# Performance work log

Measured on AMD Instinct MI355X. Metric: run time of the kernel, lower is better.

Reference implementation:

```python
import jax, jax.numpy as jnp
import numpy as np
from jax import lax

K = 3
K2 = K * K
EPS = 1e-5


def conv3x3(x, w, b=None):
    # x [B,C,H,W], w [O,C,3,3], padding=1, stride=1
    out = lax.conv_general_dilated(x, w, (1, 1), [(1, 1), (1, 1)],
                                   dimension_numbers=('NCHW', 'OIHW', 'NCHW'))
    if b is not None:
        out = out + b[None, :, None, None]
    return out


def deform_conv(x, w_off, b_off, w_mod, b_mod, w):
    # DCNv2-style deformable conv, k=3, stride=1, pad=1, dilation=1, no bias.
    B, C, H, W = x.shape
    O = w.shape[0]
    off = conv3x3(x, w_off, b_off).reshape(B, K2, 2, H, W)   # (dy,dx) per tap
    mod = 2.0 * jax.nn.sigmoid(conv3x3(x, w_mod, b_mod))      # [B,9,H,W]
    dy, dx = off[:, :, 0], off[:, :, 1]

    ky = (jnp.arange(K) - 1).astype(x.dtype)
    base_y = jnp.repeat(ky, K)   # [9]
    base_x = jnp.tile(ky, K)     # [9]
    ii = jnp.arange(H, dtype=x.dtype)[:, None]
    jj = jnp.arange(W, dtype=x.dtype)[None, :]
    py = ii[None, None] + base_y[None, :, None, None] + dy   # [B,9,H,W]
    px = jj[None, None] + base_x[None, :, None, None] + dx

    def sample(xb, pyb, pxb):
        # xb [C,H,W]; pyb/pxb [9,H,W] -> [C,9,H,W], bilinear w/ zero pad
        y0 = jnp.floor(pyb)
        x0 = jnp.floor(pxb)
        wy = pyb - y0
        wx = pxb - x0
        flat = xb.reshape(C, -1)
        acc = jnp.zeros((C, K2, H, W), xb.dtype)
        for yc, xc, wt in ((y0, x0, (1 - wy) * (1 - wx)),
                           (y0, x0 + 1, (1 - wy) * wx),
                           (y0 + 1, x0, wy * (1 - wx)),
                           (y0 + 1, x0 + 1, wy * wx)):
            yi = yc.astype(jnp.int32)
            xi = xc.astype(jnp.int32)
            valid = (yi >= 0) & (yi < H) & (xi >= 0) & (xi < W)
            idx = (jnp.clip(yi, 0, H - 1) * W + jnp.clip(xi, 0, W - 1)).reshape(-1)
            g = jnp.take(flat, idx, axis=1).reshape(C, K2, H, W)
            acc = acc + g * (wt * valid)[None]
        return acc

    patches = jax.vmap(sample)(x, py, px)          # [B,C,9,H,W]
    patches = patches * mod[:, None]               # modulated
    return jnp.einsum('bckhw,ock->bohw', patches, w.reshape(O, C, K2))


def bn_relu(x):
    # BatchNorm2d(affine=False), train-mode batch stats, biased variance
    mean = jnp.mean(x, axis=(0, 2, 3), keepdims=True)
    var = jnp.mean(jnp.square(x - mean), axis=(0, 2, 3), keepdims=True)
    return jax.nn.relu((x - mean) * lax.rsqrt(var + EPS))


def maxpool2(x):
    return lax.reduce_window(x, -jnp.inf, lax.max, (1, 1, 2, 2), (1, 1, 2, 2), 'VALID')


def setup_inputs() -> dict:
    key = jax.random.key(0)
    ks = jax.random.split(key, 11)
    B, Cin, Cout, H, W = 4, 64, 128, 128, 128
    std1 = 1.0 / np.sqrt(Cin * K2)
    std2 = 1.0 / np.sqrt(Cout * K2)
    return {
        'x': jax.random.normal(ks[0], (B, Cin, H, W), jnp.float32),
        'w_off1': jax.random.normal(ks[1], (2 * K2, Cin, K, K), jnp.float32) * 0.01,
        'b_off1': jax.random.normal(ks[2], (2 * K2,), jnp.float32) * 0.01,
        'w_mod1': jax.random.normal(ks[3], (K2, Cin, K, K), jnp.float32) * 0.01,
        'b_mod1': jnp.zeros((K2,), jnp.float32),
        'w1': jax.random.normal(ks[4], (Cout, Cin, K, K), jnp.float32) * std1,
        'w_off2': jax.random.normal(ks[5], (2 * K2, Cout, K, K), jnp.float32) * 0.01,
        'b_off2': jax.random.normal(ks[6], (2 * K2,), jnp.float32) * 0.01,
        'w_mod2': jax.random.normal(ks[7], (K2, Cout, K, K), jnp.float32) * 0.01,
        'b_mod2': jnp.zeros((K2,), jnp.float32),
        'w2': jax.random.normal(ks[8], (Cout, Cout, K, K), jnp.float32) * std2,
    }


def reference(x, w_off1, b_off1, w_mod1, b_mod1, w1,
              w_off2, b_off2, w_mod2, b_mod2, w2):
    h = bn_relu(deform_conv(x, w_off1, b_off1, w_mod1, b_mod1, w1))
    h = bn_relu(deform_conv(h, w_off2, b_off2, w_mod2, b_mod2, w2))
    return maxpool2(h)
```

## Files before the change

### kernel.cpp

```cpp
#include <hip/hip_runtime.h>
#include <math.h>

#define HH 128
#define WW 128
#define HWSZ 16384

typedef __attribute__((ext_vector_type(8))) short short8;
typedef __attribute__((ext_vector_type(4))) float f32x4;
typedef __attribute__((ext_vector_type(2))) float f32x2;
typedef unsigned short ushort;

__device__ __forceinline__ ushort f2bf(float f) {
    unsigned int u = __float_as_uint(f);
    unsigned int r = u + 0x7fffu + ((u >> 16) & 1u);
    return (ushort)(r >> 16);
}
__device__ __forceinline__ unsigned f2bf2(float lo, float hi) {
#if __has_builtin(__builtin_amdgcn_cvt_pk_bf16_f32)
    auto r = __builtin_amdgcn_cvt_pk_bf16_f32(lo, hi);
    unsigned u;
    __builtin_memcpy(&u, &r, 4);
    return u;
#else
    return (unsigned)f2bf(lo) | ((unsigned)f2bf(hi) << 16);
#endif
}
__device__ __forceinline__ f32x2 unpk(unsigned u) {
    return (f32x2){__uint_as_float(u << 16),
                   __uint_as_float(u & 0xffff0000u)};
}

__global__ __launch_bounds__(256) void prep_weights(
    const float* __restrict__ w1, const float* __restrict__ w2,
    const float* __restrict__ w_off1, const float* __restrict__ w_mod1,
    const float* __restrict__ w_off2, const float* __restrict__ w_mod2,
    ushort* __restrict__ Wt1, ushort* __restrict__ Wt2,
    ushort* __restrict__ Wo1, ushort* __restrict__ Wo2) {
    int bid = blockIdx.x, tid = threadIdx.x;
    if (bid < 336) {
        int i = bid * 256 + tid;
        int o = i / 672, kq = i % 672;
        int k = kq / 72, c = kq % 72;
        float v = (k < 9 && c < 64) ? w1[(o * 64 + c) * 9 + k] : 0.f;
        Wt1[i] = f2bf(v);
    } else if (bid < 960) {
        int i = (bid - 336) * 256 + tid;
        int o = i / 1248, kq = i % 1248;
        int k = kq / 136, c = kq % 136;
        float v = (k < 9 && c < 128) ? w2[(o * 128 + c) * 9 + k] : 0.f;
        Wt2[i] = f2bf(v);
    } else if (bid < 1032) {
        int i = (bid - 960) * 256 + tid;
        int o = i / 576, kap = i % 576;
        int k = kap / 64, c = kap % 64;
        float v = 0.f;
        if (o < 18) v = w_off1[(o * 64 + c) * 9 + k];
        else if (o < 27) v = w_mod1[((o - 18) * 64 + c) * 9 + k];
        Wo1[i] = f2bf(v);
    } else {
        int i = (bid - 1032) * 256 + tid;
        int o = i / 1152, kap = i % 1152;
        int k = kap / 128, c = kap % 128;
        float v = 0.f;
        if (o < 18) v = w_off2[(o * 128 + c) * 9 + k];
        else if (o < 27) v = w_mod2[((o - 18) * 128 + c) * 9 + k];
        Wo2[i] = f2bf(v);
    }
}

template <int C>
__global__ __launch_bounds__(256) void nhwc_cvt(const float* __restrict__ xin,
                                                unsigned* __restrict__ xout) {
    __shared__ float tile[64][C + 1];
    const int m0 = blockIdx.x * 64;
    const int b = m0 >> 14;
    const int hw0 = m0 & 16383;
    const int t = threadIdx.x;
    const int pr = t & 63, cr = t >> 6;
#pragma unroll
    for (int it = 0; it < C / 4; ++it) {
        int c = it * 4 + cr;
        tile[pr][c] = xin[(((size_t)(b * C + c)) << 14) + hw0 + pr];
    }
    __syncthreads();
    constexpr int CH = C / 2;
#pragma unroll
    for (int it = 0; it < 64 * CH / 256; ++it) {
        int slot = it * 256 + t;
        int p = slot / CH, cc = slot % CH;
        xout[(size_t)(m0 + p) * CH + cc] =
            f2bf2(tile[p][2 * cc], tile[p][2 * cc + 1]);
    }
}

template <int C>
__global__ __launch_bounds__(256) void bn_apply_cvt(
    const float* __restrict__ xin, const float* __restrict__ praw,
    unsigned* __restrict__ xout) {
    __shared__ float tile[64][C + 1];
    __shared__ float lstats[256];
    const int t = threadIdx.x;
    if (t < 128) {
        float s = 0.f, q = 0.f;
#pragma unroll
        for (int r = 0; r < 8; ++r) {
            s += praw[r * 256 + t];
            q += praw[r * 256 + 128 + t];
        }
        float mean = s / 65536.f;
        float var = q / 65536.f - mean * mean;
        lstats[t] = mean;
        lstats[128 + t] = rsqrtf(var + 1e-5f);
    }
    __syncthreads();
    const int m0 = blockIdx.x * 64;
    const int b = m0 >> 14;
    const int hw0 = m0 & 16383;
    const int pr = t & 63, cr = t >> 6;
#pragma unroll
    for (int it = 0; it < C / 4; ++it) {
        int c = it * 4 + cr;
        float v = xin[(((size_t)(b * C + c)) << 14) + hw0 + pr];
        tile[pr][c] = fmaxf(0.f, (v - lstats[c]) * lstats[C + c]);
    }
    __syncthreads();
    constexpr int CH = C / 2;
#pragma unroll
    for (int it = 0; it < 64 * CH / 256; ++it) {
        int slot = it * 256 + t;
        int p = slot / CH, cc = slot % CH;
        xout[(size_t)(m0 + p) * CH + cc] =
            f2bf2(tile[p][2 * cc], tile[p][2 * cc + 1]);
    }
}

template <int C>
__global__ __launch_bounds__(256) void offmod_nhwc(
    const ushort* __restrict__ xh, const ushort* __restrict__ wt,
    const float* __restrict__ b_off, const float* __restrict__ b_mod,
    float* __restrict__ dyb, float* __restrict__ dxb, float* __restrict__ mob,
    float* __restrict__ praw) {
    constexpr int K = C * 9;
    if (blockIdx.x < 8) praw[blockIdx.x * 256 + threadIdx.x] = 0.f;
    const int m0 = blockIdx.x * 64;
    const int b = m0 >> 14;
    const int hw0 = m0 & 16383;
    const int h = hw0 >> 7;
    const int w0 = hw0 & 127;
    const int tid = threadIdx.x;
    const int lane = tid & 63, wv = tid >> 6;
    const int n16 = lane & 15, quad = lane >> 4;
    const int p = wv * 16 + n16;
    const int w = w0 + p;

    int tbase[9];
    bool tval[9];
#pragma unroll
    for (int k = 0; k < 9; ++k) {
        int yy = h + k / 3 - 1, xx = w + k % 3 - 1;
        tval[k] = ((unsigned)yy < 128u) && ((unsigned)xx < 128u);
        int cy = min(max(yy, 0), 127), cx = min(max(xx, 0), 127);
        tbase[k] = ((b << 14) + (cy << 7) + cx) * C + quad * 8;
    }

    f32x4 acc[2];
    acc[0] = (f32x4){0.f, 0.f, 0.f, 0.f};
    acc[1] = (f32x4){0.f, 0.f, 0.f, 0.f};

    const ushort* b0p = wt + (size_t)n16 * K + quad * 8;
    const ushort* b1p = wt + (size_t)(16 + n16) * K + quad * 8;

#pragma unroll
    for (int s = 0; s < K / 32; ++s) {
        const int k = (s * 32) / C;
        const int c0 = (s * 32) % C;
        short8 a = (short8){0, 0, 0, 0, 0, 0, 0, 0};
        if (tval[k]) a = *(const short8*)(xh + (size_t)tbase[k] + c0);
        const short8 bv0 = *(const short8*)(b0p + s * 32);
        const short8 bv1 = *(const short8*)(b1p + s * 32);
        acc[0] = __builtin_amdgcn_mfma_f32_16x16x32_bf16(a, bv0, acc[0], 0, 0, 0);
        acc[1] = __builtin_amdgcn_mfma_f32_16x16x32_bf16(a, bv1, acc[1], 0, 0, 0);
    }

    __shared__ float sm[32 * 65];
#pragma unroll
    for (int nt = 0; nt < 2; ++nt) {
        int n = nt * 16 + n16;
        int pb = wv * 16 + quad * 4;
#pragma unroll
        for (int r = 0; r < 4; ++r) sm[n * 65 + pb + r] = acc[nt][r];
    }
    __syncthreads();
    {
        int n = tid >> 3, i8 = tid & 7;
        if (n < 27) {
            const float* sp = sm + n * 65 + i8 * 8;
            int px = hw0 + i8 * 8;
            if (n < 18) {
                int k = n >> 1;
                float bias = b_off[n];
                float* dst =
                    ((n & 1) ? dxb : dyb) + (((size_t)(b * 9 + k)) << 14) + px;
#pragma unroll
                for (int j = 0; j < 8; j += 4) {
                    float4 v = make_float4(sp[j] + bias, sp[j + 1] + bias,
                                           sp[j + 2] + bias, sp[j + 3] + bias);
                    *(float4*)(dst + j) = v;
                }
            } else {
                float bias = b_mod[n - 18];
                float* dst = mob + (((size_t)(b * 9 + (n - 18))) << 14) + px;
#pragma unroll
                for (int j = 0; j < 8; j += 4) {
                    float4 v;
                    v.x = 2.f / (1.f + expf(-(sp[j] + bias)));
                    v.y = 2.f / (1.f + expf(-(sp[j + 1] + bias)));
                    v.z = 2.f / (1.f + expf(-(sp[j + 2] + bias)));
                    v.w = 2.f / (1.f + expf(-(sp[j + 3] + bias)));
                    *(float4*)(dst + j) = v;
                }
            }
        }
    }
}

template <int C>
__global__ __launch_bounds__(256) void deform_mfma3(
    const ushort* __restrict__ xh, const float* __restrict__ dyb,
    const float* __restrict__ dxb, const float* __restrict__ mob,
    const ushort* __restrict__ wt, float* __restrict__ out,
    float* __restrict__ praw) {
    constexpr int PIX = 32;
    constexpr int AST = C + 8;
    constexpr int CPW = C + 8;
    constexpr int KP = ((9 * CPW + 31) / 32) * 32;
    constexpr int NCC = C / 8;
    constexpr int NIT = PIX * NCC / 256;
    constexpr int ABUF = PIX * AST;

    __shared__ __align__(16) char smem_raw[2 * ABUF * 2 + PIX * 9 * 32];
    ushort* abuf0 = (ushort*)smem_raw;
    ushort* abuf1 = abuf0 + ABUF;
    int* tb = (int*)(abuf0 + 2 * ABUF);
    float* tw = (float*)(tb + PIX * 9 * 4);

    const int m0 = blockIdx.x * PIX;
    const int b = m0 >> 14;
    const int hw0 = m0 & 16383;
    const int h = hw0 >> 7, w0 = hw0 & 127;
    const int tid = threadIdx.x;

    for (int r = tid; r < PIX * 9; r += 256) {
        int p = r & (PIX - 1), k = r / PIX;
        int oi = ((b * 9 + k) << 14) + hw0 + p;
        float py = (float)(h + k / 3 - 1) + dyb[oi];
        float px = (float)(w0 + p + k % 3 - 1) + dxb[oi];
        float mv = mob[oi];
        float y0f = floorf(py), x0f = floorf(px);
        float wy = py - y0f, wx = px - x0f;
        int y0 = (int)y0f, x0 = (int)x0f;
        int y1 = y0 + 1, x1 = x0 + 1;
        float f00 = (1.f - wy) * (1.f - wx) *
                    (((unsigned)y0 < 128u && (unsigned)x0 < 128u) ? mv : 0.f);
        float f01 = (1.f - wy) * wx *
                    (((unsigned)y0 < 128u && (unsigned)x1 < 128u) ? mv : 0.f);
        float f10 = wy * (1.f - wx) *
                    (((unsigned)y1 < 128u && (unsigned)x0 < 128u) ? mv : 0.f);
        float f11 = wy * wx *
                    (((unsigned)y1 < 128u && (unsigned)x1 < 128u) ? mv : 0.f);
        int cy0 = min(max(y0, 0), 127), cy1 = min(max(y1, 0), 127);
        int cx0 = min(max(x0, 0), 127), cx1 = min(max(x1, 0), 127);
        int bpx = b << 14;
        int s = (p * 9 + k) * 4;
        tb[s + 0] = (bpx + (cy0 << 7) + cx0) * C;
        tb[s + 1] = (bpx + (cy0 << 7) + cx1) * C;
        tb[s + 2] = (bpx + (cy1 << 7) + cx0) * C;
        tb[s + 3] = (bpx + (cy1 << 7) + cx1) * C;
        tw[s + 0] = f00;
        tw[s + 1] = f01;
        tw[s + 2] = f10;
        tw[s + 3] = f11;
    }
    __syncthreads();

    auto issue_loads = [&](int kc, uint4 (&q)[2][4], float4 (&fw)[2]) {
#pragma unroll
        for (int it = 0; it < NIT; ++it) {
            int e = it * 256 + tid;
            int p = e / NCC, cc = e % NCC;
            int s = (p * 9 + kc) * 4;
            int4 bi = *(const int4*)&tb[s];
            fw[it] = *(const float4*)&tw[s];
            q[it][0] = *(const uint4*)(xh + (size_t)bi.x + cc * 8);
            q[it][1] = *(const uint4*)(xh + (size_t)bi.y + cc * 8);
            q[it][2] = *(const uint4*)(xh + (size_t)bi.z + cc * 8);
            q[it][3] = *(const uint4*)(xh + (size_t)bi.w + cc * 8);
        }
    };
    auto interp_write = [&](ushort* dst, uint4 (&q)[2][4], float4 (&fw)[2]) {
#pragma unroll
        for (int it = 0; it < NIT; ++it) {
            int e = it * 256 + tid;
            int p = e / NCC, cc = e % NCC;
            unsigned a0[4] = {q[it][0].x, q[it][0].y, q[it][0].z, q[it][0].w};
            unsigned a1[4] = {q[it][1].x, q[it][1].y, q[it][1].z, q[it][1].w};
            unsigned a2[4] = {q[it][2].x, q[it][2].y, q[it][2].z, q[it][2].w};
            unsigned a3[4] = {q[it][3].x, q[it][3].y, q[it][3].z, q[it][3].w};
            unsigned ov[4];
#pragma unroll
            for (int dw = 0; dw < 4; ++dw) {
                f32x2 v = unpk(a0[dw]) * fw[it].x;
                v += unpk(a1[dw]) * fw[it].y;
                v += unpk(a2[dw]) * fw[it].z;
                v += unpk(a3[dw]) * fw[it].w;
                ov[dw] = f2bf2(v.x, v.y);
            }
            *(uint4*)&dst[p * AST + cc * 8] = uint4{ov[0], ov[1], ov[2], ov[3]};
        }
    };

    {
        uint4 q[2][4];
        float4 fw[2];
        issue_loads(0, q, fw);
        interp_write(abuf0, q, fw);
    }
    __syncthreads();

    const int lane = tid & 63, wv = tid >> 6;
    const int n16 = lane & 15, quad = lane >> 4;

    f32x4 acc[2][2];
#pragma unroll
    for (int mt = 0; mt < 2; ++mt)
#pragma unroll
        for (int nt = 0; nt < 2; ++nt) acc[mt][nt] = (f32x4){0.f, 0.f, 0.f, 0.f};

    const ushort* bbase[2];
#pragma unroll
    for (int nt = 0; nt < 2; ++nt)
        bbase[nt] = wt + (size_t)(wv * 32 + nt * 16 + n16) * KP + quad * 8;

#pragma unroll 1
    for (int kc = 0; kc < 9; ++kc) {
        uint4 q[2][4];
        float4 fw[2];
        if (kc < 8) issue_loads(kc + 1, q, fw);

        const ushort* ab = (kc & 1) ? abuf1 : abuf0;
#pragma unroll
        for (int s = 0; s < C / 32; ++s) {
            short8 av[2], bv[2];
#pragma unroll
            for (int mt = 0; mt < 2; ++mt)
                av[mt] = *(const short8*)(ab + (mt * 16 + n16) * AST + s * 32 +
                                          quad * 8);
#pragma unroll
            for (int nt = 0; nt < 2; ++nt)
                bv[nt] = *(const short8*)(bbase[nt] + kc * CPW + s * 32);
#pragma unroll
            for (int mt = 0; mt < 2; ++mt)
#pragma unroll
                for (int nt = 0; nt < 2; ++nt)
                    acc[mt][nt] = __builtin_amdgcn_mfma_f32_16x16x32_bf16(
                        av[mt], bv[nt], acc[mt][nt], 0, 0, 0);
        }
        if (kc < 8)
            interp_write((kc & 1) ? abuf0 : abuf1, q, fw);
        __syncthreads();
    }

    float* sm = (float*)smem_raw;
    constexpr int SROW = PIX + 1;
#pragma unroll
    for (int mt = 0; mt < 2; ++mt)
#pragma unroll
        for (int nt = 0; nt < 2; ++nt) {
            int o = wv * 32 + nt * 16 + n16;
            int mb = mt * 16 + quad * 4;
#pragma unroll
            for (int r = 0; r < 4; ++r) sm[o * SROW + mb + r] = acc[mt][nt][r];
        }
    __syncthreads();
    {
        int o = tid >> 1, half = tid & 1;
        constexpr int HP = PIX / 2;
        const float* sp = sm + o * SROW + half * HP;
        float* op = out + (((size_t)(b * 128 + o)) << 14) + hw0 + half * HP;
        float s = 0.f, qq = 0.f;
#pragma unroll
        for (int i = 0; i < HP; i += 4) {
            float4 v = make_float4(sp[i], sp[i + 1], sp[i + 2], sp[i + 3]);
            *(float4*)(op + i) = v;
            s += v.x + v.y + v.z + v.w;
            qq += v.x * v.x + v.y * v.y + v.z * v.z + v.w * v.w;
        }
        s += __shfl_down(s, 1, 64);
        qq += __shfl_down(qq, 1, 64);
        if (half == 0) {
            float* pr = praw + (blockIdx.x & 7) * 256;
            atomicAdd(&pr[o], s);
            atomicAdd(&pr[128 + o], qq);
        }
    }
}

__global__ __launch_bounds__(256) void bn_pool(const float* __restrict__ x,
                                               const float* __restrict__ praw,
                                               float* __restrict__ out, int B,
                                               int C) {
    __shared__ float lstats[256];
    if (threadIdx.x < 128) {
        int c = threadIdx.x;
        float s = 0.f, q = 0.f;
#pragma unroll
        for (int r = 0; r < 8; ++r) {
            s += praw[r * 256 + c];
            q += praw[r * 256 + 128 + c];
        }
        float mean = s / 65536.f;
        float var = q / 65536.f - mean * mean;
        lstats[c] = mean;
        lstats[128 + c] = rsqrtf(var + 1e-5f);
    }
    __syncthreads();
    const int Ho = 64, Wo = 64;
    int i = blockIdx.x * blockDim.x + threadIdx.x;
    int total = B * C * Ho * Wo;
    if (i >= total) return;
    int ow = i % Wo;
    int t = i / Wo;
    int oh = t % Ho;
    t /= Ho;
    int c = t % C;
    int b = t / C;
    const float* p = x + ((size_t)(b * C + c)) * HWSZ + (2 * oh) * WW + 2 * ow;
    float m0 = fmaxf(p[0], p[1]);
    float m1 = fmaxf(p[WW], p[WW + 1]);
    float mx = fmaxf(m0, m1);
    out[i] = fmaxf(0.f, (mx - lstats[c]) * lstats[C + c]);
}

extern "C" void kernel_launch(void* const* d_in, const int* in_sizes, int n_in,
                              void* d_out, int out_size, void* d_ws,
                              size_t ws_size, hipStream_t stream) {
    (void)in_sizes;
    (void)n_in;
    (void)out_size;
    (void)ws_size;
    const float* x = (const float*)d_in[0];
    const float* w_off1 = (const float*)d_in[1];
    const float* b_off1 = (const float*)d_in[2];
    const float* w_mod1 = (const float*)d_in[3];
    const float* b_mod1 = (const float*)d_in[4];
    const float* w1 = (const float*)d_in[5];
    const float* w_off2 = (const float*)d_in[6];
    const float* b_off2 = (const float*)d_in[7];
    const float* w_mod2 = (const float*)d_in[8];
    const float* b_mod2 = (const float*)d_in[9];
    const float* w2 = (const float*)d_in[10];
    float* out = (float*)d_out;
    float* ws = (float*)d_ws;

    ushort* Wt1 = (ushort*)ws;
    ushort* Wt2 = (ushort*)(ws + 43008);
    ushort* Wo1 = (ushort*)(ws + 43008 + 79872);
    ushort* Wo2 = (ushort*)(ws + 43008 + 79872 + 16384);
    float* dyb = ws + 172032;
    float* dxb = dyb + 589824;
    float* mob = dxb + 589824;
    float* hbuf = mob + 589824;
    float* xhf = hbuf + 8388608;
    float* h1hf = xhf + 2097152;
    float* praw = h1hf + 4194304;
    ushort* xh = (ushort*)xhf;
    ushort* h1h = (ushort*)h1hf;

    prep_weights<<<1176, 256, 0, stream>>>(w1, w2, w_off1, w_mod1, w_off2,
                                           w_mod2, Wt1, Wt2, Wo1, Wo2);

    nhwc_cvt<64><<<1024, 256, 0, stream>>>(x, (unsigned*)xh);
    offmod_nhwc<64><<<1024, 256, 0, stream>>>(xh, Wo1, b_off1, b_mod1, dyb, dxb,
                                              mob, praw);
    deform_mfma3<64><<<2048, 256, 0, stream>>>(xh, dyb, dxb, mob, Wt1, hbuf,
                                               praw);
    bn_apply_cvt<128><<<1024, 256, 0, stream>>>(hbuf, praw, (unsigned*)h1h);

    offmod_nhwc<128><<<1024, 256, 0, stream>>>(h1h, Wo2, b_off2, b_mod2, dyb,
                                               dxb, mob, praw);
    deform_mfma3<128><<<2048, 256, 0, stream>>>(h1h, dyb, dxb, mob, Wt2, hbuf,
                                                praw);
    bn_pool<<<8192, 256, 0, stream>>>(hbuf, praw, out, 4, 128);
}
```

Before: 294.7 us.

## Fuse 2x2 max-pool into second deformable conv epilogue before BN normalization

The second deformable conv kernel now tiles each block as 2 rows by 16 columns, so it can max-pool 2x2 windows in its epilogue. It writes only the pooled pre-normalization values while still accumulating the BN statistics from the full-resolution outputs. A lightweight kernel then applies the normalization and ReLU to the pooled tensor, relying on max-pool commuting with a monotone positive-scale BN plus ReLU. This removes the full-resolution intermediate write and read, at the cost of a different pixel tile shape for the gathers.

```diff
diff --git a/kernel.cpp b/kernel.cpp
--- a/kernel.cpp
+++ b/kernel.cpp
@@ -405,10 +405,199 @@
     }
 }
 
-__global__ __launch_bounds__(256) void bn_pool(const float* __restrict__ x,
-                                               const float* __restrict__ praw,
-                                               float* __restrict__ out, int B,
-                                               int C) {
+template <int C>
+__global__ __launch_bounds__(256) void deform_mfma3p(
+    const ushort* __restrict__ xh, const float* __restrict__ dyb,
+    const float* __restrict__ dxb, const float* __restrict__ mob,
+    const ushort* __restrict__ wt, float* __restrict__ pout,
+    float* __restrict__ praw) {
+    constexpr int PIX = 32;
+    constexpr int AST = C + 8;
+    constexpr int CPW = C + 8;
+    constexpr int KP = ((9 * CPW + 31) / 32) * 32;
+    constexpr int NCC = C / 8;
+    constexpr int NIT = PIX * NCC / 256;
+    constexpr int ABUF = PIX * AST;
+
+    __shared__ __align__(16) char smem_raw[2 * ABUF * 2 + PIX * 9 * 32];
+    ushort* abuf0 = (ushort*)smem_raw;
+    ushort* abuf1 = abuf0 + ABUF;
+    int* tb = (int*)(abuf0 + 2 * ABUF);
+    float* tw = (float*)(tb + PIX * 9 * 4);
+
+    const int bid = blockIdx.x;
+    const int b = bid >> 9;
+    const int rp = (bid >> 3) & 63;
+    const int g = bid & 7;
+    const int tid = threadIdx.x;
+
+    for (int r = tid; r < PIX * 9; r += 256) {
+        int p = r & (PIX - 1), k = r / PIX;
+        int row = 2 * rp + (p >> 4), col = g * 16 + (p & 15);
+        int oi = ((b * 9 + k) << 14) + (row << 7) + col;
+        float py = (float)(row + k / 3 - 1) + dyb[oi];
+        float px = (float)(col + k % 3 - 1) + dxb[oi];
+        float mv = mob[oi];
+        float y0f = floorf(py), x0f = floorf(px);
+        float wy = py - y0f, wx = px - x0f;
+        int y0 = (int)y0f, x0 = (int)x0f;
+        int y1 = y0 + 1, x1 = x0 + 1;
+        float f00 = (1.f - wy) * (1.f - wx) *
+                    (((unsigned)y0 < 128u && (unsigned)x0 < 128u) ? mv : 0.f);
+        float f01 = (1.f - wy) * wx *
+                    (((unsigned)y0 < 128u && (unsigned)x1 < 128u) ? mv : 0.f);
+        float f10 = wy * (1.f - wx) *
+                    (((unsigned)y1 < 128u && (unsigned)x0 < 128u) ? mv : 0.f);
+        float f11 = wy * wx *
+                    (((unsigned)y1 < 128u && (unsigned)x1 < 128u) ? mv : 0.f);
+        int cy0 = min(max(y0, 0), 127), cy1 = min(max(y1, 0), 127);
+        int cx0 = min(max(x0, 0), 127), cx1 = min(max(x1, 0), 127);
+        int bpx = b << 14;
+        int s = (p * 9 + k) * 4;
+        tb[s + 0] = (bpx + (cy0 << 7) + cx0) * C;
+        tb[s + 1] = (bpx + (cy0 << 7) + cx1) * C;
+        tb[s + 2] = (bpx + (cy1 << 7) + cx0) * C;
+        tb[s + 3] = (bpx + (cy1 << 7) + cx1) * C;
+        tw[s + 0] = f00;
+        tw[s + 1] = f01;
+        tw[s + 2] = f10;
+        tw[s + 3] = f11;
+    }
+    __syncthreads();
+
+    auto issue_loads = [&](int kc, uint4 (&q)[2][4], float4 (&fw)[2]) {
+#pragma unroll
+        for (int it = 0; it < NIT; ++it) {
+            int e = it * 256 + tid;
+            int p = e / NCC, cc = e % NCC;
+            int s = (p * 9 + kc) * 4;
+            int4 bi = *(const int4*)&tb[s];
+            fw[it] = *(const float4*)&tw[s];
+            q[it][0] = *(const uint4*)(xh + (size_t)bi.x + cc * 8);
+            q[it][1] = *(const uint4*)(xh + (size_t)bi.y + cc * 8);
+            q[it][2] = *(const uint4*)(xh + (size_t)bi.z + cc * 8);
+            q[it][3] = *(const uint4*)(xh + (size_t)bi.w + cc * 8);
+        }
+    };
+    auto interp_write = [&](ushort* dst, uint4 (&q)[2][4], float4 (&fw)[2]) {
+#pragma unroll
+        for (int it = 0; it < NIT; ++it) {
+            int e = it * 256 + tid;
+            int p = e / NCC, cc = e % NCC;
+            unsigned a0[4] = {q[it][0].x, q[it][0].y, q[it][0].z, q[it][0].w};
+            unsigned a1[4] = {q[it][1].x, q[it][1].y, q[it][1].z, q[it][1].w};
+            unsigned a2[4] = {q[it][2].x, q[it][2].y, q[it][2].z, q[it][2].w};
+            unsigned a3[4] = {q[it][3].x, q[it][3].y, q[it][3].z, q[it][3].w};
+            unsigned ov[4];
+#pragma unroll
+            for (int dw = 0; dw < 4; ++dw) {
+                f32x2 v = unpk(a0[dw]) * fw[it].x;
+                v += unpk(a1[dw]) * fw[it].y;
+                v += unpk(a2[dw]) * fw[it].z;
+                v += unpk(a3[dw]) * fw[it].w;
+                ov[dw] = f2bf2(v.x, v.y);
+            }
+            *(uint4*)&dst[p * AST + cc * 8] = uint4{ov[0], ov[1], ov[2], ov[3]};
+        }
+    };
+
+    {
+        uint4 q[2][4];
+        float4 fw[2];
+        issue_loads(0, q, fw);
+        interp_write(abuf0, q, fw);
+    }
+    __syncthreads();
+
+    const int lane = tid & 63, wv = tid >> 6;
+    const int n16 = lane & 15, quad = lane >> 4;
+
+    f32x4 acc[2][2];
+#pragma unroll
+    for (int mt = 0; mt < 2; ++mt)
+#pragma unroll
+        for (int nt = 0; nt < 2; ++nt) acc[mt][nt] = (f32x4){0.f, 0.f, 0.f, 0.f};
+
+    const ushort* bbase[2];
+#pragma unroll
+    for (int nt = 0; nt < 2; ++nt)
+        bbase[nt] = wt + (size_t)(wv * 32 + nt * 16 + n16) * KP + quad * 8;
+
+#pragma unroll 1
+    for (int kc = 0; kc < 9; ++kc) {
+        uint4 q[2][4];
+        float4 fw[2];
+        if (kc < 8) issue_loads(kc + 1, q, fw);
+
+        const ushort* ab = (kc & 1) ? abuf1 : abuf0;
+#pragma unroll
+        for (int s = 0; s < C / 32; ++s) {
+            short8 av[2], bv[2];
+#pragma unroll
+            for (int mt = 0; mt < 2; ++mt)
+                av[mt] = *(const short8*)(ab + (mt * 16 + n16) * AST + s * 32 +
+                                          quad * 8);
+#pragma unroll
+            for (int nt = 0; nt < 2; ++nt)
+                bv[nt] = *(const short8*)(bbase[nt] + kc * CPW + s * 32);
+#pragma unroll
+            for (int mt = 0; mt < 2; ++mt)
+#pragma unroll
+                for (int nt = 0; nt < 2; ++nt)
+                    acc[mt][nt] = __builtin_amdgcn_mfma_f32_16x16x32_bf16(
+                        av[mt], bv[nt], acc[mt][nt], 0, 0, 0);
+        }
+        if (kc < 8)
+            interp_write((kc & 1) ? abuf0 : abuf1, q, fw);
+        __syncthreads();
+    }
+
+    float* sm = (float*)smem_raw;
+    constexpr int SROW = PIX + 1;
+#pragma unroll
+    for (int mt = 0; mt < 2; ++mt)
+#pragma unroll
+        for (int nt = 0; nt < 2; ++nt) {
+            int o = wv * 32 + nt * 16 + n16;
+            int mb = mt * 16 + quad * 4;
+#pragma unroll
+            for (int r = 0; r < 4; ++r) sm[o * SROW + mb + r] = acc[mt][nt][r];
+        }
+    __syncthreads();
+    {
+        int o = tid >> 1, half = tid & 1;
+        const float* so = sm + o * SROW;
+        const float* sp = so + half * 16;
+        float s = 0.f, qq = 0.f;
+#pragma unroll
+        for (int i = 0; i < 16; i += 4) {
+            float4 v = make_float4(sp[i], sp[i + 1], sp[i + 2], sp[i + 3]);
+            s += v.x + v.y + v.z + v.w;
+            qq += v.x * v.x + v.y * v.y + v.z * v.z + v.w * v.w;
+        }
+        s += __shfl_down(s, 1, 64);
+        qq += __shfl_down(qq, 1, 64);
+        if (half == 0) {
+            float* pr = praw + (blockIdx.x & 7) * 256;
+            atomicAdd(&pr[o], s);
+            atomicAdd(&pr[128 + o], qq);
+        }
+        float4 pv;
+#pragma unroll
+        for (int i = 0; i < 4; ++i) {
+            int pc = half * 4 + i;
+            float m0v = fmaxf(so[2 * pc], so[2 * pc + 1]);
+            float m1v = fmaxf(so[16 + 2 * pc], so[16 + 2 * pc + 1]);
+            ((float*)&pv)[i] = fmaxf(m0v, m1v);
+        }
+        *(float4*)(pout + (((size_t)(b * 128 + o)) << 12) + rp * 64 + g * 8 +
+                   half * 4) = pv;
+    }
+}
+
+__global__ __launch_bounds__(256) void pool_norm(const float* __restrict__ pout,
+                                                 const float* __restrict__ praw,
+                                                 float* __restrict__ out) {
     __shared__ float lstats[256];
     if (threadIdx.x < 128) {
         int c = threadIdx.x;
@@ -424,21 +613,15 @@
         lstats[128 + c] = rsqrtf(var + 1e-5f);
     }
     __syncthreads();
-    const int Ho = 64, Wo = 64;
-    int i = blockIdx.x * blockDim.x + threadIdx.x;
-    int total = B * C * Ho * Wo;
-    if (i >= total) return;
-    int ow = i % Wo;
-    int t = i / Wo;
-    int oh = t % Ho;
-    t /= Ho;
-    int c = t % C;
-    int b = t / C;
-    const float* p = x + ((size_t)(b * C + c)) * HWSZ + (2 * oh) * WW + 2 * ow;
-    float m0 = fmaxf(p[0], p[1]);
-    float m1 = fmaxf(p[WW], p[WW + 1]);
-    float mx = fmaxf(m0, m1);
-    out[i] = fmaxf(0.f, (mx - lstats[c]) * lstats[C + c]);
+    int i = blockIdx.x * 256 + threadIdx.x;
+    int c = (i >> 10) & 127;
+    float mean = lstats[c], rstd = lstats[128 + c];
+    float4 v = ((const float4*)pout)[i];
+    v.x = fmaxf(0.f, (v.x - mean) * rstd);
+    v.y = fmaxf(0.f, (v.y - mean) * rstd);
+    v.z = fmaxf(0.f, (v.z - mean) * rstd);
+    v.w = fmaxf(0.f, (v.w - mean) * rstd);
+    ((float4*)out)[i] = v;
 }
 
 extern "C" void kernel_launch(void* const* d_in, const int* in_sizes, int n_in,
@@ -488,7 +671,7 @@
 
     offmod_nhwc<128><<<1024, 256, 0, stream>>>(h1h, Wo2, b_off2, b_mod2, dyb,
                                                dxb, mob, praw);
-    deform_mfma3<128><<<2048, 256, 0, stream>>>(h1h, dyb, dxb, mob, Wt2, hbuf,
-                                                praw);
-    bn_pool<<<8192, 256, 0, stream>>>(hbuf, praw, out, 4, 128);
-}
+    deform_mfma3p<128><<<2048, 256, 0, stream>>>(h1h, dyb, dxb, mob, Wt2, hbuf,
+                                                 praw);
+    pool_norm<<<2048, 256, 0, stream>>>(hbuf, praw, out);
+}
```

Measured after the change: 287.7 us. 1.02x faster.
